# Optimization experiments

Hardware: AMD Instinct MI355X
Metric: run time of the kernel (lower is better)

Reference implementation:

```python
import jax, jax.numpy as jnp
import numpy as np
from jax import lax

MAX_ITERS = 200
X_INNER_ITERS = 20
RHO = 1.0
X_STEP = 1e-3


def setup_inputs() -> dict:
    key = jax.random.key(0)
    k1, k2, k3 = jax.random.split(key, 3)
    m, n = 512, 1024
    # Scale A so x_step * rho * ||A^T A||_2 < 2 -> inner GD loop is stable.
    A = jax.random.normal(k1, (m, n), dtype=jnp.float32) / jnp.sqrt(jnp.float32(n))
    b = jax.random.normal(k2, (m,), dtype=jnp.float32)
    c = jax.random.normal(k3, (n,), dtype=jnp.float32)
    return {"A": A, "b": b, "c": c}


def _admm(A, b, c):
    m, n = A.shape
    x0 = jnp.zeros((n,), dtype=A.dtype)
    s0 = jnp.zeros((m,), dtype=A.dtype)
    u0 = jnp.zeros((m,), dtype=A.dtype)

    def outer_step(carry, _):
        x, s, u = carry
        r = s + b - u  # [m]

        def inner_step(xk, _):
            grad = c + RHO * (A.T @ (A @ xk - r))  # [n]
            xk = jnp.maximum(xk - X_STEP * grad, 0.0)
            return xk, None

        x, _ = lax.scan(inner_step, x, None, length=X_INNER_ITERS)
        Ax = A @ x  # [m]
        s = jnp.maximum(Ax - b + u, 0.0)
        u = u + (Ax - s - b)
        return (x, s, u), None

    (x, s, u), _ = lax.scan(outer_step, (x0, s0, u0), None, length=MAX_ITERS)
    p = RHO * u
    lambda_k = jnp.maximum(-p, 0.0)          # [m]
    nu_k = jnp.maximum(c + A.T @ p, 0.0)     # [n]
    return x, s, u, lambda_k, nu_k


def reference(A, b, c):
    # return_history=False, so x_hist is None in the original; omitted here.
    return _admm(A, b, c)
```

## Files before the change

### kernel.cpp

```cpp
#include <hip/hip_runtime.h>

#define MDIM 512
#define NDIM 1024
#define MAX_OUTER 200
#define X_INNER 20
#define RHO 1.0f
#define XSTEP 1e-3f

#define GBLK 32
#define TPB 256
#define NPER (NDIM / GBLK)
#define MPER (MDIM / GBLK)


__device__ __forceinline__ float agent_load(const float* p) {
  return __hip_atomic_load(p, __ATOMIC_RELAXED, __HIP_MEMORY_SCOPE_AGENT);
}
__device__ __forceinline__ void agent_store(float* p, float v) {
  __hip_atomic_store(p, v, __ATOMIC_RELAXED, __HIP_MEMORY_SCOPE_AGENT);
}

__device__ __forceinline__ float wave_reduce_sum(float v) {
#pragma unroll
  for (int off = 32; off > 0; off >>= 1) v += __shfl_xor(v, off, 64);
  return v;
}

__device__ __forceinline__ void grid_barrier(int* flags, int epoch, int bid) {
  __syncthreads();
  if (threadIdx.x == 0)
    __hip_atomic_store(&flags[bid * 32], epoch, __ATOMIC_RELEASE,
                       __HIP_MEMORY_SCOPE_AGENT);
  if (threadIdx.x < GBLK) {
    while (__hip_atomic_load(&flags[threadIdx.x * 32], __ATOMIC_RELAXED,
                             __HIP_MEMORY_SCOPE_AGENT) < epoch) {
    }
  }
  __syncthreads();
  __builtin_amdgcn_fence(__ATOMIC_ACQUIRE, "agent");
}


#define ATA_BK 32
#define ATA_BT 64

__global__ void __launch_bounds__(256) ata_kernel(const float* __restrict__ A,
                                                  float* __restrict__ Mout) {
  __shared__ float As[ATA_BK][ATA_BT];
  __shared__ float Bs[ATA_BK][ATA_BT];
  const int bi = blockIdx.y * ATA_BT;
  const int bj = blockIdx.x * ATA_BT;
  const int tid = threadIdx.x;
  const int tx = tid & 15, ty = tid >> 4;
  float acc[4][4] = {};
  for (int k0 = 0; k0 < MDIM; k0 += ATA_BK) {
#pragma unroll
    for (int t = tid; t < ATA_BK * ATA_BT; t += 256) {
      int kk = t >> 6, ii = t & 63;
      As[kk][ii] = A[(size_t)(k0 + kk) * NDIM + bi + ii];
      Bs[kk][ii] = A[(size_t)(k0 + kk) * NDIM + bj + ii];
    }
    __syncthreads();
#pragma unroll
    for (int kk = 0; kk < ATA_BK; ++kk) {
      float a[4], bb[4];
#pragma unroll
      for (int r = 0; r < 4; ++r) a[r] = As[kk][ty * 4 + r];
#pragma unroll
      for (int r = 0; r < 4; ++r) bb[r] = Bs[kk][tx * 4 + r];
#pragma unroll
      for (int r = 0; r < 4; ++r)
#pragma unroll
        for (int q = 0; q < 4; ++q) acc[r][q] = fmaf(a[r], bb[q], acc[r][q]);
    }
    __syncthreads();
  }
#pragma unroll
  for (int r = 0; r < 4; ++r)
#pragma unroll
    for (int q = 0; q < 4; ++q)
      Mout[(size_t)(bi + ty * 4 + r) * NDIM + bj + tx * 4 + q] = acc[r][q];
}


__global__ void __launch_bounds__(TPB) admm_kernel(
    const float* __restrict__ A, const float* __restrict__ bvec,
    const float* __restrict__ cvec, const float* __restrict__ Mm,
    float* __restrict__ xg0, float* __restrict__ xg1, float* __restrict__ sg,
    float* __restrict__ ug, int* flags, float* __restrict__ out) {
  __shared__ float4 Ml4[NPER][NDIM / 4];
  __shared__ float rs[MDIM];
  __shared__ float wl[NPER];
  __shared__ float cl[NPER];
  __shared__ float wred[NPER][9];

  const int tid = threadIdx.x;
  const int bid = blockIdx.x;
  const int wave = tid >> 6;
  const int lane = tid & 63;
  const int i0 = bid * NPER;
  const int k0 = bid * MPER;

  {
    const float4* Msrc = (const float4*)(Mm + (size_t)i0 * NDIM);
    float4* Mdst = &Ml4[0][0];
    for (int f = tid; f < NPER * NDIM / 4; f += TPB) Mdst[f] = Msrc[f];
  }
  if (tid < NPER) cl[tid] = cvec[i0 + tid];

  float xr[4][4];
#pragma unroll
  for (int t = 0; t < 4; ++t)
#pragma unroll
    for (int q = 0; q < 4; ++q) xr[t][q] = 0.0f;
  float ox[8];
#pragma unroll
  for (int r = 0; r < 8; ++r) ox[r] = 0.0f;

  float* xa = xg0;
  float* xb = xg1;
  int epoch = 0;
  __syncthreads();

  for (int outer = 0; outer < MAX_OUTER; ++outer) {
    for (int k = tid; k < MDIM; k += TPB)
      rs[k] = agent_load(&sg[k]) + bvec[k] - agent_load(&ug[k]);
    __syncthreads();
    {
      const int ii = tid & (NPER - 1);
      const int kg = tid >> 5;
      float pp = 0.0f;
#pragma unroll
      for (int kk = 0; kk < MDIM / 8; ++kk) {
        const int k = kg * (MDIM / 8) + kk;
        pp = fmaf(A[(size_t)k * NDIM + i0 + ii], rs[k], pp);
      }
      wred[ii][kg] = pp;
    }
    __syncthreads();
    if (tid < NPER) {
      float sum = 0.0f;
#pragma unroll
      for (int q = 0; q < 8; ++q) sum += wred[tid][q];
      wl[tid] = sum;
    }
    __syncthreads();

    for (int it = 0; it < X_INNER; ++it) {
      float acc[8];
#pragma unroll
      for (int r = 0; r < 8; ++r) acc[r] = 0.0f;
#pragma unroll
      for (int r = 0; r < 8; ++r) {
        const int rl = wave * 8 + r;
#pragma unroll
        for (int t = 0; t < 4; ++t) {
          const float4 m = Ml4[rl][lane + 64 * t];
          acc[r] = fmaf(m.x, xr[t][0], acc[r]);
          acc[r] = fmaf(m.y, xr[t][1], acc[r]);
          acc[r] = fmaf(m.z, xr[t][2], acc[r]);
          acc[r] = fmaf(m.w, xr[t][3], acc[r]);
        }
      }
#pragma unroll
      for (int r = 0; r < 8; ++r) acc[r] = wave_reduce_sum(acc[r]);
      if (lane == 0) {
#pragma unroll
        for (int r = 0; r < 8; ++r) {
          const int ii = wave * 8 + r;
          const float g = cl[ii] + RHO * (acc[r] - wl[ii]);
          const float xn = fmaxf(ox[r] - XSTEP * g, 0.0f);
          ox[r] = xn;
          agent_store(&xb[i0 + ii], xn);
        }
      }
      ++epoch;
      grid_barrier(flags, epoch, bid);
#pragma unroll
      for (int t = 0; t < 4; ++t)
#pragma unroll
        for (int q = 0; q < 4; ++q)
          xr[t][q] = agent_load(&xb[4 * lane + 256 * t + q]);
      float* tmp = xa;
      xa = xb;
      xb = tmp;
    }

#pragma unroll
    for (int r = 0; r < 4; ++r) {
      const int k = k0 + wave * 4 + r;
      const float4* Arow4 = (const float4*)(A + (size_t)k * NDIM);
      float pp = 0.0f;
#pragma unroll
      for (int t = 0; t < 4; ++t) {
        const float4 a = Arow4[lane + 64 * t];
        pp = fmaf(a.x, xr[t][0], pp);
        pp = fmaf(a.y, xr[t][1], pp);
        pp = fmaf(a.z, xr[t][2], pp);
        pp = fmaf(a.w, xr[t][3], pp);
      }
      pp = wave_reduce_sum(pp);
      if (lane == 0) {
        const float uk = agent_load(&ug[k]);
        const float bk = bvec[k];
        const float sv = fmaxf(pp - bk + uk, 0.0f);
        agent_store(&sg[k], sv);
        agent_store(&ug[k], uk + pp - sv - bk);
      }
    }
    ++epoch;
    grid_barrier(flags, epoch, bid);
  }

  if (tid < NPER) out[i0 + tid] = agent_load(&xa[i0 + tid]);
  if (tid < MPER) {
    const int k = k0 + tid;
    const float sv = agent_load(&sg[k]);
    const float uv = agent_load(&ug[k]);
    out[NDIM + k] = sv;
    out[NDIM + MDIM + k] = uv;
    out[NDIM + 2 * MDIM + k] = fmaxf(-RHO * uv, 0.0f);
  }
  for (int k = tid; k < MDIM; k += TPB) rs[k] = agent_load(&ug[k]);
  __syncthreads();
  {
    const int ii = tid & (NPER - 1);
    const int kg = tid >> 5;
    float pp = 0.0f;
#pragma unroll
    for (int kk = 0; kk < MDIM / 8; ++kk) {
      const int k = kg * (MDIM / 8) + kk;
      pp = fmaf(A[(size_t)k * NDIM + i0 + ii], rs[k], pp);
    }
    wred[ii][kg] = pp;
  }
  __syncthreads();
  if (tid < NPER) {
    float t = 0.0f;
#pragma unroll
    for (int q = 0; q < 8; ++q) t += wred[tid][q];
    out[NDIM + 3 * MDIM + i0 + tid] = fmaxf(cl[tid] + RHO * t, 0.0f);
  }
}


extern "C" void kernel_launch(void* const* d_in, const int* in_sizes, int n_in,
                              void* d_out, int out_size, void* d_ws,
                              size_t ws_size, hipStream_t stream) {
  const float* A = (const float*)d_in[0];
  const float* b = (const float*)d_in[1];
  const float* c = (const float*)d_in[2];
  float* out = (float*)d_out;

  float* Mws = (float*)d_ws;
  float* xg0 = Mws + (size_t)NDIM * NDIM;
  float* xg1 = xg0 + NDIM;
  float* sg = xg1 + NDIM;
  float* ug = sg + MDIM;
  int* flags = (int*)(ug + MDIM);

  hipMemsetAsync(xg0, 0,
                 (2 * NDIM + 2 * MDIM) * sizeof(float) +
                     GBLK * 32 * sizeof(int),
                 stream);

  dim3 g1(NDIM / ATA_BT, NDIM / ATA_BT);
  ata_kernel<<<g1, 256, 0, stream>>>(A, Mws);
  admm_kernel<<<GBLK, TPB, 0, stream>>>(A, b, c, Mws, xg0, xg1, sg, ug, flags,
                                        out);
}
```

Measured before the change: 23.09 ms.

## Replicate Ax/s/u update per block to drop a grid barrier per outer step

Each block now recomputes the full A·x product and the s/u updates locally, keeping s and u in shared memory instead of global buffers. This removes the grid-wide barrier after the s/u update in every outer iteration. The barrier flags are packed contiguously with a sleep in the spin loop, and the x exchange uses 64-bit atomic loads and stores. In exchange every block reads all of A each outer iteration, which adds redundant L2 traffic and compute.

```diff
diff --git a/kernel.cpp b/kernel.cpp
--- a/kernel.cpp
+++ b/kernel.cpp
@@ -16,8 +16,22 @@
 __device__ __forceinline__ float agent_load(const float* p) {
   return __hip_atomic_load(p, __ATOMIC_RELAXED, __HIP_MEMORY_SCOPE_AGENT);
 }
-__device__ __forceinline__ void agent_store(float* p, float v) {
-  __hip_atomic_store(p, v, __ATOMIC_RELAXED, __HIP_MEMORY_SCOPE_AGENT);
+__device__ __forceinline__ unsigned long long agent_load8(const void* p) {
+  return __hip_atomic_load((const unsigned long long*)p, __ATOMIC_RELAXED,
+                           __HIP_MEMORY_SCOPE_AGENT);
+}
+__device__ __forceinline__ void agent_store8(void* p, unsigned long long v) {
+  __hip_atomic_store((unsigned long long*)p, v, __ATOMIC_RELAXED,
+                     __HIP_MEMORY_SCOPE_AGENT);
+}
+__device__ __forceinline__ unsigned long long pk2(float a, float b) {
+  union {
+    float f[2];
+    unsigned long long u;
+  } c;
+  c.f[0] = a;
+  c.f[1] = b;
+  return c.u;
 }
 
 __device__ __forceinline__ float wave_reduce_sum(float v) {
@@ -29,12 +43,12 @@
 __device__ __forceinline__ void grid_barrier(int* flags, int epoch, int bid) {
   __syncthreads();
   if (threadIdx.x == 0)
-    __hip_atomic_store(&flags[bid * 32], epoch, __ATOMIC_RELEASE,
+    __hip_atomic_store(&flags[bid], epoch, __ATOMIC_RELEASE,
                        __HIP_MEMORY_SCOPE_AGENT);
   if (threadIdx.x < GBLK) {
-    while (__hip_atomic_load(&flags[threadIdx.x * 32], __ATOMIC_RELAXED,
-                             __HIP_MEMORY_SCOPE_AGENT) < epoch) {
-    }
+    while (__hip_atomic_load(&flags[threadIdx.x], __ATOMIC_RELAXED,
+                             __HIP_MEMORY_SCOPE_AGENT) < epoch)
+      __builtin_amdgcn_s_sleep(1);
   }
   __syncthreads();
   __builtin_amdgcn_fence(__ATOMIC_ACQUIRE, "agent");
@@ -86,10 +100,12 @@
 __global__ void __launch_bounds__(TPB) admm_kernel(
     const float* __restrict__ A, const float* __restrict__ bvec,
     const float* __restrict__ cvec, const float* __restrict__ Mm,
-    float* __restrict__ xg0, float* __restrict__ xg1, float* __restrict__ sg,
-    float* __restrict__ ug, int* flags, float* __restrict__ out) {
+    float* __restrict__ xg0, float* __restrict__ xg1, int* flags,
+    float* __restrict__ out) {
   __shared__ float4 Ml4[NPER][NDIM / 4];
   __shared__ float rs[MDIM];
+  __shared__ float sl[MDIM];
+  __shared__ float ul[MDIM];
   __shared__ float wl[NPER];
   __shared__ float cl[NPER];
   __shared__ float wred[NPER][9];
@@ -107,12 +123,14 @@
     for (int f = tid; f < NPER * NDIM / 4; f += TPB) Mdst[f] = Msrc[f];
   }
   if (tid < NPER) cl[tid] = cvec[i0 + tid];
-
-  float xr[4][4];
-#pragma unroll
-  for (int t = 0; t < 4; ++t)
-#pragma unroll
-    for (int q = 0; q < 4; ++q) xr[t][q] = 0.0f;
+  for (int k = tid; k < MDIM; k += TPB) {
+    sl[k] = 0.0f;
+    ul[k] = 0.0f;
+  }
+
+  float4 xr[4];
+#pragma unroll
+  for (int t = 0; t < 4; ++t) xr[t] = make_float4(0.f, 0.f, 0.f, 0.f);
   float ox[8];
 #pragma unroll
   for (int r = 0; r < 8; ++r) ox[r] = 0.0f;
@@ -123,8 +141,7 @@
   __syncthreads();
 
   for (int outer = 0; outer < MAX_OUTER; ++outer) {
-    for (int k = tid; k < MDIM; k += TPB)
-      rs[k] = agent_load(&sg[k]) + bvec[k] - agent_load(&ug[k]);
+    for (int k = tid; k < MDIM; k += TPB) rs[k] = sl[k] + bvec[k] - ul[k];
     __syncthreads();
     {
       const int ii = tid & (NPER - 1);
@@ -152,76 +169,82 @@
       for (int r = 0; r < 8; ++r) acc[r] = 0.0f;
 #pragma unroll
       for (int r = 0; r < 8; ++r) {
-        const int rl = wave * 8 + r;
+        const float4* Mr = Ml4[wave * 8 + r];
 #pragma unroll
         for (int t = 0; t < 4; ++t) {
-          const float4 m = Ml4[rl][lane + 64 * t];
-          acc[r] = fmaf(m.x, xr[t][0], acc[r]);
-          acc[r] = fmaf(m.y, xr[t][1], acc[r]);
-          acc[r] = fmaf(m.z, xr[t][2], acc[r]);
-          acc[r] = fmaf(m.w, xr[t][3], acc[r]);
+          const float4 m = Mr[64 * t + lane];
+          acc[r] = fmaf(m.x, xr[t].x, acc[r]);
+          acc[r] = fmaf(m.y, xr[t].y, acc[r]);
+          acc[r] = fmaf(m.z, xr[t].z, acc[r]);
+          acc[r] = fmaf(m.w, xr[t].w, acc[r]);
         }
       }
 #pragma unroll
       for (int r = 0; r < 8; ++r) acc[r] = wave_reduce_sum(acc[r]);
+#pragma unroll
+      for (int r = 0; r < 8; ++r) {
+        const int ii = wave * 8 + r;
+        const float g = cl[ii] + RHO * (acc[r] - wl[ii]);
+        ox[r] = fmaxf(ox[r] - XSTEP * g, 0.0f);
+      }
       if (lane == 0) {
-#pragma unroll
-        for (int r = 0; r < 8; ++r) {
-          const int ii = wave * 8 + r;
-          const float g = cl[ii] + RHO * (acc[r] - wl[ii]);
-          const float xn = fmaxf(ox[r] - XSTEP * g, 0.0f);
-          ox[r] = xn;
-          agent_store(&xb[i0 + ii], xn);
-        }
+        float* dst = &xb[i0 + wave * 8];
+        agent_store8(dst + 0, pk2(ox[0], ox[1]));
+        agent_store8(dst + 2, pk2(ox[2], ox[3]));
+        agent_store8(dst + 4, pk2(ox[4], ox[5]));
+        agent_store8(dst + 6, pk2(ox[6], ox[7]));
       }
       ++epoch;
       grid_barrier(flags, epoch, bid);
 #pragma unroll
-      for (int t = 0; t < 4; ++t)
-#pragma unroll
-        for (int q = 0; q < 4; ++q)
-          xr[t][q] = agent_load(&xb[4 * lane + 256 * t + q]);
+      for (int t = 0; t < 4; ++t) {
+        union {
+          unsigned long long u[2];
+          float f[4];
+        } cv;
+        const unsigned long long* p8 =
+            (const unsigned long long*)&xb[4 * (64 * t + lane)];
+        cv.u[0] = agent_load8(p8);
+        cv.u[1] = agent_load8(p8 + 1);
+        xr[t] = make_float4(cv.f[0], cv.f[1], cv.f[2], cv.f[3]);
+      }
       float* tmp = xa;
       xa = xb;
       xb = tmp;
     }
 
-#pragma unroll
-    for (int r = 0; r < 4; ++r) {
-      const int k = k0 + wave * 4 + r;
-      const float4* Arow4 = (const float4*)(A + (size_t)k * NDIM);
+    for (int rr = 0; rr < 128; ++rr) {
+      const int k = wave * 128 + rr;
+      const float4* Ar = (const float4*)(A + (size_t)k * NDIM);
       float pp = 0.0f;
 #pragma unroll
       for (int t = 0; t < 4; ++t) {
-        const float4 a = Arow4[lane + 64 * t];
-        pp = fmaf(a.x, xr[t][0], pp);
-        pp = fmaf(a.y, xr[t][1], pp);
-        pp = fmaf(a.z, xr[t][2], pp);
-        pp = fmaf(a.w, xr[t][3], pp);
+        const float4 a = Ar[64 * t + lane];
+        pp = fmaf(a.x, xr[t].x, pp);
+        pp = fmaf(a.y, xr[t].y, pp);
+        pp = fmaf(a.z, xr[t].z, pp);
+        pp = fmaf(a.w, xr[t].w, pp);
       }
       pp = wave_reduce_sum(pp);
       if (lane == 0) {
-        const float uk = agent_load(&ug[k]);
-        const float bk = bvec[k];
+        const float uk = ul[k], bk = bvec[k];
         const float sv = fmaxf(pp - bk + uk, 0.0f);
-        agent_store(&sg[k], sv);
-        agent_store(&ug[k], uk + pp - sv - bk);
-      }
-    }
-    ++epoch;
-    grid_barrier(flags, epoch, bid);
+        sl[k] = sv;
+        ul[k] = uk + pp - sv - bk;
+      }
+    }
+    __syncthreads();
   }
 
   if (tid < NPER) out[i0 + tid] = agent_load(&xa[i0 + tid]);
   if (tid < MPER) {
     const int k = k0 + tid;
-    const float sv = agent_load(&sg[k]);
-    const float uv = agent_load(&ug[k]);
+    const float sv = sl[k], uv = ul[k];
     out[NDIM + k] = sv;
     out[NDIM + MDIM + k] = uv;
     out[NDIM + 2 * MDIM + k] = fmaxf(-RHO * uv, 0.0f);
   }
-  for (int k = tid; k < MDIM; k += TPB) rs[k] = agent_load(&ug[k]);
+  for (int k = tid; k < MDIM; k += TPB) rs[k] = ul[k];
   __syncthreads();
   {
     const int ii = tid & (NPER - 1);
@@ -255,17 +278,12 @@
   float* Mws = (float*)d_ws;
   float* xg0 = Mws + (size_t)NDIM * NDIM;
   float* xg1 = xg0 + NDIM;
-  float* sg = xg1 + NDIM;
-  float* ug = sg + MDIM;
-  int* flags = (int*)(ug + MDIM);
-
-  hipMemsetAsync(xg0, 0,
-                 (2 * NDIM + 2 * MDIM) * sizeof(float) +
-                     GBLK * 32 * sizeof(int),
+  int* flags = (int*)(xg1 + NDIM);
+
+  hipMemsetAsync(xg0, 0, 2 * NDIM * sizeof(float) + GBLK * sizeof(int),
                  stream);
 
   dim3 g1(NDIM / ATA_BT, NDIM / ATA_BT);
   ata_kernel<<<g1, 256, 0, stream>>>(A, Mws);
-  admm_kernel<<<GBLK, TPB, 0, stream>>>(A, b, c, Mws, xg0, xg1, sg, ug, flags,
-                                        out);
-}
+  admm_kernel<<<GBLK, TPB, 0, stream>>>(A, b, c, Mws, xg0, xg1, flags, out);
+}
```

Result: slower. 39.70 ms (+72.0%).
